# Optimization experiments

Measured on AMD Instinct MI355X. Metric: run time of the kernel, lower is better.

## Reference

```python
import jax, jax.numpy as jnp
import numpy as np

NUM_CLASSES = 9
TEMP = 0.1
ALPHA = 0.99
EPS = 1e-12  # F.normalize default eps


def _l2norm(x, axis=-1):
    n = jnp.linalg.norm(x, axis=axis, keepdims=True)
    return x / jnp.maximum(n, EPS)


def setup_inputs() -> dict:
    key = jax.random.key(0)
    k1, k2, k3, k4, k5 = jax.random.split(key, 5)
    B, D, h, w = 4, 768, 128, 128
    return {
        "cls_score": jax.random.normal(k1, (B, NUM_CLASSES, h, w), dtype=jnp.float32),
        "label": jax.random.randint(k2, (B, 4 * h, 4 * w), 0, NUM_CLASSES, dtype=jnp.int64),
        "gt_lucas": jax.random.randint(k3, (B, 4 * h, 4 * w), 0, NUM_CLASSES, dtype=jnp.int64),
        "features": jax.random.normal(k4, (B, D, h, w), dtype=jnp.float32),
        "prototypes": jax.random.uniform(k5, (NUM_CLASSES, D), dtype=jnp.float32),
    }


def reference(cls_score, label, gt_lucas, features, prototypes):
    B, D, h, w = features.shape
    # so the masked gathers reduce to a full flatten (static shapes).
    corine = label[:, ::4, ::4].reshape(-1)          # [N]
    lucas = gt_lucas[:, ::4, ::4].reshape(-1)        # [N] (mask trivially all valid)
    feats = jnp.transpose(features, (0, 2, 3, 1)).reshape(-1, D)  # [N, D]
    N = feats.shape[0]
    # note: original indexes corine labels under the lucas mask (mask all-true here)
    labels_lucas = corine
    labels_corine = jnp.where(corine == 7, 6, corine)
    # per-class EMA prototype update (unique(labels_lucas) == arange(9) by construction;
    # compute_ema detaches the new mean)
    sums = jax.ops.segment_sum(feats, labels_lucas, num_segments=NUM_CLASSES)      # [C, D]
    counts = jax.ops.segment_sum(jnp.ones((N,), feats.dtype), labels_lucas,
                                 num_segments=NUM_CLASSES)                          # [C]
    means = jax.lax.stop_gradient(sums / counts[:, None])
    protos = ALPHA * means + (1.0 - ALPHA) * prototypes
    protos = _l2norm(protos, axis=-1)                # F.normalize over feature dim
    logits = protos @ feats.T                        # [C, N]
    prot_feat = _l2norm(logits, axis=-1) / TEMP      # normalize each class row over N
    prot_feat = prot_feat.at[2].set((labels_corine == 2).astype(prot_feat.dtype))
    E = jnp.exp(prot_feat)                           # [C, N]
    A1 = E[labels_corine, jnp.arange(N)]             # [N]
    A2 = E.sum(axis=0)                               # [N]
    return jnp.mean(-jnp.log(A1 / A2))
```

## Files before the change

kernel.cpp:

```cpp
#include <hip/hip_runtime.h>
#include <math.h>

#define NCLS 9
#define DIM 768
#define NPIX 65536

#define OFF_LAB     ((size_t)0)
#define OFF_HIST    ((size_t)65536)
#define OFF_SUMS    ((size_t)74752)
#define OFF_SUMSQ   ((size_t)102400)
#define OFF_LOSS    ((size_t)102464)
#define OFF_DONE    ((size_t)102480)
#define OFF_PROTO   ((size_t)102528)
#define OFF_LOGITS  ((size_t)139392)

__device__ __forceinline__ float waveReduceSum(float v) {
#pragma unroll
  for (int off = 32; off > 0; off >>= 1) v += __shfl_down(v, off, 64);
  return v;
}

__global__ void k0_lab(const int* __restrict__ label, unsigned char* __restrict__ lab,
                       int* __restrict__ hist, float* __restrict__ sumsq,
                       float* __restrict__ lossacc, unsigned int* __restrict__ done) {
  __shared__ int h[NCLS];
  int tid = threadIdx.x;
  if (tid < NCLS) h[tid] = 0;
  __syncthreads();
  int n = blockIdx.x * 256 + tid;
  int b = n >> 14, r = (n >> 7) & 127, cc = n & 127;
  int c = label[b * 262144 + r * 2048 + cc * 4];
  lab[n] = (unsigned char)c;
  atomicAdd(&h[c], 1);
  if (blockIdx.x == 0) {
    if (tid < 16) sumsq[tid] = 0.f;
    else if (tid == 16) lossacc[0] = 0.f;
    else if (tid == 17) done[0] = 0u;
  }
  __syncthreads();
  if (tid < NCLS) hist[blockIdx.x * NCLS + tid] = h[tid];
}

__global__ void k1_segsum(const float4* __restrict__ feat4, const uchar4* __restrict__ lab4,
                          float* __restrict__ sums) {
  int d = blockIdx.x;
  int tid = threadIdx.x;
  float acc[NCLS];
#pragma unroll
  for (int k = 0; k < NCLS; ++k) acc[k] = 0.f;
  for (int b = 0; b < 4; ++b) {
    const float4* fp = feat4 + (size_t)(b * DIM + d) * 4096;
    const uchar4* lp = lab4 + b * 4096;
#pragma unroll 4
    for (int i = 0; i < 16; ++i) {
      int p = tid + i * 256;
      float4 f = fp[p];
      uchar4 l = lp[p];
      int lx = l.x, ly = l.y, lz = l.z, lw = l.w;
#pragma unroll
      for (int k = 0; k < NCLS; ++k) {
        acc[k] += (lx == k) ? f.x : 0.f;
        acc[k] += (ly == k) ? f.y : 0.f;
        acc[k] += (lz == k) ? f.z : 0.f;
        acc[k] += (lw == k) ? f.w : 0.f;
      }
    }
  }
  __shared__ float red[4][NCLS];
#pragma unroll
  for (int k = 0; k < NCLS; ++k) acc[k] = waveReduceSum(acc[k]);
  int lane = tid & 63, w = tid >> 6;
  if (lane == 0) {
#pragma unroll
    for (int k = 0; k < NCLS; ++k) red[w][k] = acc[k];
  }
  __syncthreads();
  if (tid < NCLS)
    sums[tid * DIM + d] = red[0][tid] + red[1][tid] + red[2][tid] + red[3][tid];
}

__global__ void k2_proto(const float* __restrict__ sums, const int* __restrict__ hist,
                         const float* __restrict__ proto, float* __restrict__ protoT) {
  __shared__ float red[12][NCLS];
  __shared__ float inv[NCLS];
  __shared__ float cpart[16][NCLS];
  __shared__ float cnt[NCLS];
  int tid = threadIdx.x;
  if (tid < 144) {
    int c = tid % NCLS, g = tid / NCLS;
    int s = 0;
#pragma unroll
    for (int j = 0; j < 16; ++j) s += hist[(g * 16 + j) * NCLS + c];
    cpart[g][c] = (float)s;
  }
  __syncthreads();
  if (tid < NCLS) {
    float s = 0.f;
#pragma unroll
    for (int g = 0; g < 16; ++g) s += cpart[g][tid];
    cnt[tid] = s;
  }
  __syncthreads();
  float v[NCLS];
#pragma unroll
  for (int c = 0; c < NCLS; ++c)
    v[c] = 0.99f * (sums[c * DIM + tid] / cnt[c]) + 0.01f * proto[c * DIM + tid];
  int lane = tid & 63, w = tid >> 6;
#pragma unroll
  for (int c = 0; c < NCLS; ++c) {
    float q = waveReduceSum(v[c] * v[c]);
    if (lane == 0) red[w][c] = q;
  }
  __syncthreads();
  if (tid < NCLS) {
    float t = 0.f;
#pragma unroll
    for (int w2 = 0; w2 < 12; ++w2) t += red[w2][tid];
    inv[tid] = 1.f / fmaxf(sqrtf(t), 1e-12f);
  }
  __syncthreads();
#pragma unroll
  for (int c = 0; c < NCLS; ++c) protoT[tid * 12 + c] = v[c] * inv[c];
}

__global__ void __launch_bounds__(1024) k3_logits(const float* __restrict__ feat,
                                                  const float* __restrict__ protoT,
                                                  float* __restrict__ logits,
                                                  float* __restrict__ sumsq) {
  __shared__ float pl[4 * 2304];
  __shared__ float red2[2][NCLS];
  int tid = threadIdx.x;
  int grp = __builtin_amdgcn_readfirstlane(tid >> 7);
  int g = tid & 127;
  int n0 = blockIdx.x * 256;
  int b = n0 >> 14, ppb = n0 & 16383;
  const float* fr = feat + ((size_t)(b * DIM + grp * 96)) * 16384 + ppb + g;
  const float* pp = protoT + grp * 96 * 12;
  float a[NCLS][2];
#pragma unroll
  for (int c = 0; c < NCLS; ++c) { a[c][0] = 0.f; a[c][1] = 0.f; }

#pragma unroll 4
  for (int dd = 0; dd < 96; ++dd) {
    float f0 = fr[0], f1 = fr[128];
    float4 q0 = *(const float4*)pp;
    float4 q1 = *(const float4*)(pp + 4);
    float q8 = pp[8];
    float pcs[NCLS] = {q0.x, q0.y, q0.z, q0.w, q1.x, q1.y, q1.z, q1.w, q8};
#pragma unroll
    for (int c = 0; c < NCLS; ++c) {
      a[c][0] += pcs[c] * f0;
      a[c][1] += pcs[c] * f1;
    }
    fr += 16384;
    pp += 12;
  }
  __syncthreads();

  if (grp >= 4) {
    float* rp = pl + (size_t)(grp - 4) * 2304 + g;
#pragma unroll
    for (int c = 0; c < NCLS; ++c) {
      rp[c * 256] = a[c][0];
      rp[c * 256 + 128] = a[c][1];
    }
  }
  __syncthreads();
  if (grp < 4) {
    const float* rp = pl + (size_t)grp * 2304 + g;
#pragma unroll
    for (int c = 0; c < NCLS; ++c) {
      a[c][0] += rp[c * 256];
      a[c][1] += rp[c * 256 + 128];
    }
  }
  __syncthreads();
  if (grp >= 1 && grp < 4) {
    float* rp = pl + (size_t)(grp - 1) * 2304 + g;
#pragma unroll
    for (int c = 0; c < NCLS; ++c) {
      rp[c * 256] = a[c][0];
      rp[c * 256 + 128] = a[c][1];
    }
  }
  __syncthreads();
  if (grp == 0) {
#pragma unroll
    for (int q = 0; q < 3; ++q) {
      const float* rp = pl + (size_t)q * 2304 + g;
#pragma unroll
      for (int c = 0; c < NCLS; ++c) {
        a[c][0] += rp[c * 256];
        a[c][1] += rp[c * 256 + 128];
      }
    }
    float ss[NCLS];
#pragma unroll
    for (int c = 0; c < NCLS; ++c) {
      logits[(size_t)c * NPIX + n0 + g] = a[c][0];
      logits[(size_t)c * NPIX + n0 + 128 + g] = a[c][1];
      ss[c] = waveReduceSum(a[c][0] * a[c][0] + a[c][1] * a[c][1]);
    }
    int lane = tid & 63, w = tid >> 6;
    if (lane == 0) {
#pragma unroll
      for (int c = 0; c < NCLS; ++c) red2[w][c] = ss[c];
    }
  }
  __syncthreads();
  if (tid < NCLS) atomicAdd(&sumsq[tid], red2[0][tid] + red2[1][tid]);
}

__global__ void k5_loss(const float4* __restrict__ logits4, const uchar4* __restrict__ lab4,
                        const float* __restrict__ sumsq, float* __restrict__ lossacc,
                        unsigned int* __restrict__ done, float* __restrict__ out) {
  int t = blockIdx.x * 256 + threadIdx.x;
  int tid = threadIdx.x;
  float scale[NCLS];
#pragma unroll
  for (int c = 0; c < NCLS; ++c) scale[c] = 10.f / fmaxf(sqrtf(sumsq[c]), 1e-12f);
  float arr[NCLS][4];
#pragma unroll
  for (int c = 0; c < NCLS; ++c) {
    float4 v = logits4[(size_t)c * 16384 + t];
    arr[c][0] = v.x; arr[c][1] = v.y; arr[c][2] = v.z; arr[c][3] = v.w;
  }
  uchar4 lb = lab4[t];
  int lv[4] = {lb.x, lb.y, lb.z, lb.w};
  float lsum = 0.f;
#pragma unroll
  for (int j = 0; j < 4; ++j) {
    int l = lv[j];
    int lc = (l == 7) ? 6 : l;
    float sumE = 0.f, picked = 0.f;
#pragma unroll
    for (int c = 0; c < NCLS; ++c) {
      float pf = (c == 2) ? ((lc == 2) ? 1.f : 0.f) : arr[c][j] * scale[c];
      sumE += __expf(pf);
      picked += (c == lc) ? pf : 0.f;
    }
    lsum += __logf(sumE) - picked;
  }
  lsum = waveReduceSum(lsum);
  __shared__ float red[4];
  int lane = tid & 63, w = tid >> 6;
  if (lane == 0) red[w] = lsum;
  __syncthreads();
  if (tid == 0) {
    atomicAdd(lossacc, red[0] + red[1] + red[2] + red[3]);
    __threadfence();
    unsigned int ticket = atomicAdd(done, 1u);
    if (ticket == gridDim.x - 1) {
      __threadfence();
      float total = __hip_atomic_load(lossacc, __ATOMIC_ACQUIRE, __HIP_MEMORY_SCOPE_AGENT);
      out[0] = total * (1.f / (float)NPIX);
    }
  }
}

extern "C" void kernel_launch(void* const* d_in, const int* in_sizes, int n_in,
                              void* d_out, int out_size, void* d_ws, size_t ws_size,
                              hipStream_t stream) {
  const int* label = (const int*)d_in[1];
  const float* feat = (const float*)d_in[3];
  const float* proto = (const float*)d_in[4];
  char* ws = (char*)d_ws;
  unsigned char* lab = (unsigned char*)(ws + OFF_LAB);
  int* hist = (int*)(ws + OFF_HIST);
  float* sums = (float*)(ws + OFF_SUMS);
  float* sumsq = (float*)(ws + OFF_SUMSQ);
  float* lossacc = (float*)(ws + OFF_LOSS);
  unsigned int* done = (unsigned int*)(ws + OFF_DONE);
  float* protoT = (float*)(ws + OFF_PROTO);
  float* logits = (float*)(ws + OFF_LOGITS);

  k0_lab<<<NPIX / 256, 256, 0, stream>>>(label, lab, hist, sumsq, lossacc, done);
  k1_segsum<<<DIM, 256, 0, stream>>>((const float4*)feat, (const uchar4*)lab, sums);
  k2_proto<<<1, 768, 0, stream>>>(sums, hist, proto, protoT);
  k3_logits<<<NPIX / 256, 1024, 0, stream>>>(feat, protoT, logits, sumsq);
  k5_loss<<<64, 256, 0, stream>>>((const float4*)logits, (const uchar4*)lab, sumsq, lossacc,
                                  done, (float*)d_out);
}
```

Baseline: 110.0 us.

## Split logits GEMV over feature dim into global partials plus combine kernel

Replaces the 1024-thread logits kernel, which reduced eight feature-dim slices through shared memory in a block, with a split-K kernel. There, each of 512 blocks handles one 96-wide slice of D for 1024 pixels and writes partial logits to a global workspace. A new combine kernel sums the 8 partials, writes the logits and accumulates the per-class sum of squares. It also stages the prototype slice in LDS. This removes the multi-stage barrier reduction and improves per-block occupancy, but adds about 19 MB of extra global partial writes and reads plus one more launch.

```diff
diff --git a/kernel.cpp b/kernel.cpp
--- a/kernel.cpp
+++ b/kernel.cpp
@@ -4,6 +4,7 @@
 #define NCLS 9
 #define DIM 768
 #define NPIX 65536
+#define NSPLIT 8
 
 #define OFF_LAB     ((size_t)0)
 #define OFF_HIST    ((size_t)65536)
@@ -13,6 +14,7 @@
 #define OFF_DONE    ((size_t)102480)
 #define OFF_PROTO   ((size_t)102528)
 #define OFF_LOGITS  ((size_t)139392)
+#define OFF_PART    ((size_t)2498688)
 
 __device__ __forceinline__ float waveReduceSum(float v) {
 #pragma unroll
@@ -123,26 +125,26 @@
   for (int c = 0; c < NCLS; ++c) protoT[tid * 12 + c] = v[c] * inv[c];
 }
 
-__global__ void __launch_bounds__(1024) k3_logits(const float* __restrict__ feat,
-                                                  const float* __restrict__ protoT,
-                                                  float* __restrict__ logits,
-                                                  float* __restrict__ sumsq) {
-  __shared__ float pl[4 * 2304];
-  __shared__ float red2[2][NCLS];
-  int tid = threadIdx.x;
-  int grp = __builtin_amdgcn_readfirstlane(tid >> 7);
-  int g = tid & 127;
-  int n0 = blockIdx.x * 256;
-  int b = n0 >> 14, ppb = n0 & 16383;
-  const float* fr = feat + ((size_t)(b * DIM + grp * 96)) * 16384 + ppb + g;
-  const float* pp = protoT + grp * 96 * 12;
+__global__ void __launch_bounds__(512) k3_splitk(const float* __restrict__ feat,
+                                                 const float* __restrict__ protoT,
+                                                 float* __restrict__ part) {
+  __shared__ float pl[96 * 12];
+  int tid = threadIdx.x;
+  int g = blockIdx.x >> 6;
+  int t = blockIdx.x & 63;
+  if (tid < 288) ((float4*)pl)[tid] = ((const float4*)protoT)[g * 288 + tid];
+  __syncthreads();
+
+  int b = t >> 4, pb = (t & 15) * 1024;
+  const float* fr = feat + ((size_t)(b * DIM + g * 96)) * 16384 + pb + tid;
+  const float* pp = pl;
   float a[NCLS][2];
 #pragma unroll
   for (int c = 0; c < NCLS; ++c) { a[c][0] = 0.f; a[c][1] = 0.f; }
 
 #pragma unroll 4
   for (int dd = 0; dd < 96; ++dd) {
-    float f0 = fr[0], f1 = fr[128];
+    float f0 = fr[0], f1 = fr[512];
     float4 q0 = *(const float4*)pp;
     float4 q1 = *(const float4*)(pp + 4);
     float q8 = pp[8];
@@ -155,60 +157,42 @@
     fr += 16384;
     pp += 12;
   }
-  __syncthreads();
-
-  if (grp >= 4) {
-    float* rp = pl + (size_t)(grp - 4) * 2304 + g;
-#pragma unroll
-    for (int c = 0; c < NCLS; ++c) {
-      rp[c * 256] = a[c][0];
-      rp[c * 256 + 128] = a[c][1];
-    }
-  }
-  __syncthreads();
-  if (grp < 4) {
-    const float* rp = pl + (size_t)grp * 2304 + g;
-#pragma unroll
-    for (int c = 0; c < NCLS; ++c) {
-      a[c][0] += rp[c * 256];
-      a[c][1] += rp[c * 256 + 128];
-    }
-  }
-  __syncthreads();
-  if (grp >= 1 && grp < 4) {
-    float* rp = pl + (size_t)(grp - 1) * 2304 + g;
-#pragma unroll
-    for (int c = 0; c < NCLS; ++c) {
-      rp[c * 256] = a[c][0];
-      rp[c * 256 + 128] = a[c][1];
-    }
-  }
-  __syncthreads();
-  if (grp == 0) {
-#pragma unroll
-    for (int q = 0; q < 3; ++q) {
-      const float* rp = pl + (size_t)q * 2304 + g;
-#pragma unroll
-      for (int c = 0; c < NCLS; ++c) {
-        a[c][0] += rp[c * 256];
-        a[c][1] += rp[c * 256 + 128];
-      }
-    }
-    float ss[NCLS];
-#pragma unroll
-    for (int c = 0; c < NCLS; ++c) {
-      logits[(size_t)c * NPIX + n0 + g] = a[c][0];
-      logits[(size_t)c * NPIX + n0 + 128 + g] = a[c][1];
-      ss[c] = waveReduceSum(a[c][0] * a[c][0] + a[c][1] * a[c][1]);
-    }
-    int lane = tid & 63, w = tid >> 6;
-    if (lane == 0) {
-#pragma unroll
-      for (int c = 0; c < NCLS; ++c) red2[w][c] = ss[c];
-    }
-  }
-  __syncthreads();
-  if (tid < NCLS) atomicAdd(&sumsq[tid], red2[0][tid] + red2[1][tid]);
+
+  float* op = part + ((size_t)g * NCLS) * NPIX + t * 1024 + tid;
+#pragma unroll
+  for (int c = 0; c < NCLS; ++c) {
+    op[(size_t)c * NPIX] = a[c][0];
+    op[(size_t)c * NPIX + 512] = a[c][1];
+  }
+}
+
+__global__ void k4_combine(const float4* __restrict__ part4, float4* __restrict__ logits4,
+                           float* __restrict__ sumsq) {
+  int t = blockIdx.x * 256 + threadIdx.x;
+  int tid = threadIdx.x;
+  float ssq[NCLS];
+#pragma unroll
+  for (int c = 0; c < NCLS; ++c) {
+    float4 v = part4[(size_t)(0 * NCLS + c) * 16384 + t];
+#pragma unroll
+    for (int s = 1; s < NSPLIT; ++s) {
+      float4 wv = part4[(size_t)(s * NCLS + c) * 16384 + t];
+      v.x += wv.x; v.y += wv.y; v.z += wv.z; v.w += wv.w;
+    }
+    logits4[(size_t)c * 16384 + t] = v;
+    ssq[c] = v.x * v.x + v.y * v.y + v.z * v.z + v.w * v.w;
+  }
+  __shared__ float red[4][NCLS];
+#pragma unroll
+  for (int c = 0; c < NCLS; ++c) ssq[c] = waveReduceSum(ssq[c]);
+  int lane = tid & 63, w = tid >> 6;
+  if (lane == 0) {
+#pragma unroll
+    for (int c = 0; c < NCLS; ++c) red[w][c] = ssq[c];
+  }
+  __syncthreads();
+  if (tid < NCLS)
+    atomicAdd(&sumsq[tid], red[0][tid] + red[1][tid] + red[2][tid] + red[3][tid]);
 }
 
 __global__ void k5_loss(const float4* __restrict__ logits4, const uchar4* __restrict__ lab4,
@@ -273,11 +257,13 @@
   unsigned int* done = (unsigned int*)(ws + OFF_DONE);
   float* protoT = (float*)(ws + OFF_PROTO);
   float* logits = (float*)(ws + OFF_LOGITS);
+  float* part = (float*)(ws + OFF_PART);
 
   k0_lab<<<NPIX / 256, 256, 0, stream>>>(label, lab, hist, sumsq, lossacc, done);
   k1_segsum<<<DIM, 256, 0, stream>>>((const float4*)feat, (const uchar4*)lab, sums);
   k2_proto<<<1, 768, 0, stream>>>(sums, hist, proto, protoT);
-  k3_logits<<<NPIX / 256, 1024, 0, stream>>>(feat, protoT, logits, sumsq);
+  k3_splitk<<<NSPLIT * 64, 512, 0, stream>>>(feat, protoT, part);
+  k4_combine<<<64, 256, 0, stream>>>((const float4*)part, (float4*)logits, sumsq);
   k5_loss<<<64, 256, 0, stream>>>((const float4*)logits, (const uchar4*)lab, sumsq, lossacc,
                                   done, (float*)d_out);
 }
```

Measured after the change: 112.1 us. No clear change (+1.9%).
